# Kernel optimization log

Measured on AMD Instinct MI355X. Metric: run time of the kernel, lower is better.

Reference implementation:

```python
import math
import jax, jax.numpy as jnp
import numpy as np

E = 1024   # embed_dim
H = 16     # num_heads
DH = E // H
EPS = 1e-8

def round_ste(x):
    # straight-through round (matches brevitas STE behavior)
    return x + jax.lax.stop_gradient(jnp.round(x) - x)

def _scale(x, qmax):
    # dynamic per-tensor abs-max scale (stand-in for brevitas calibrated scale)
    return jnp.maximum(jnp.max(jnp.abs(x)) / qmax, EPS)

def fq(x, s, qmin, qmax):
    # fake-quantize: quantize to int grid, dequantize back to float
    return jnp.clip(round_ste(x / s), qmin, qmax) * s

def quant_linear(x, W, b):
    # Int8ActPerTensorFloat input, Int8WeightPerTensorFloat (narrow range) weight, Int32Bias
    s_x = _scale(x, 128.0)
    s_w = _scale(W, 127.0)
    xq = fq(x, s_x, -128, 127)
    wq = fq(W, s_w, -127, 127)
    y = xq @ wq.T
    if b is not None:
        s_b = s_x * s_w
        y = y + round_ste(b / s_b) * s_b
    return y

def setup_inputs() -> dict:
    k = jax.random.key(0)
    ks = jax.random.split(k, 7)
    S, B = 1024, 4
    return {
        "query": jax.random.normal(ks[0], (S, B, E), jnp.float32),
        "key": jax.random.normal(ks[1], (S, B, E), jnp.float32),
        "value": jax.random.normal(ks[2], (S, B, E), jnp.float32),
        "in_proj_weight": jax.random.normal(ks[3], (3 * E, E), jnp.float32) * 0.02,
        "in_proj_bias": jax.random.normal(ks[4], (3 * E,), jnp.float32) * 0.02,
        "out_proj_weight": jax.random.normal(ks[5], (E, E), jnp.float32) * 0.02,
        "out_proj_bias": jax.random.normal(ks[6], (E,), jnp.float32) * 0.02,
    }

def reference(query, key, value, in_proj_weight, in_proj_bias, out_proj_weight, out_proj_bias):
    S, B, _ = query.shape
    Wq, Wk, Wv = jnp.split(in_proj_weight, 3, axis=0)
    bq, bk, bv = jnp.split(in_proj_bias, 3)
    # quantized QKV projections (packed in_proj split per-input)
    q = quant_linear(query, Wq, bq)   # (S,B,E)
    k = quant_linear(key, Wk, bk)
    v = quant_linear(value, Wv, bv)

    def to_heads(x):  # (S,B,E) -> (B*H, S, DH)
        return x.reshape(S, B * H, DH).transpose(1, 0, 2)

    q = to_heads(q)
    k = to_heads(k)
    v = to_heads(v)

    # q_scaled quant (int8)
    q = q / math.sqrt(DH)
    q = fq(q, _scale(q, 128.0), -128, 127)
    # k_transposed quant (int8)
    kt = k.transpose(0, 2, 1)  # (B*H, DH, S)
    kt = fq(kt, _scale(kt, 128.0), -128, 127)

    attn = q @ kt                      # (B*H, S, S); softmax_input_quant=None -> identity
    attn = jax.nn.softmax(attn, axis=-1)
    # attn_output_weights quant (uint8)
    s_a = jnp.maximum(jnp.max(attn) / 255.0, EPS)
    attn = jnp.clip(round_ste(attn / s_a), 0, 255) * s_a
    # v quant (int8)
    v = fq(v, _scale(v, 128.0), -128, 127)

    out = attn @ v                     # (B*H, S, DH)
    out = out.transpose(1, 0, 2).reshape(S, B, E)
    out = quant_linear(out, out_proj_weight, out_proj_bias)
    return out
```

## Files before the change

### kernel.cpp

```cpp
#include <hip/hip_runtime.h>
#include <stdint.h>

typedef unsigned short u16;
typedef signed char i8;
typedef unsigned char u8;
typedef __attribute__((ext_vector_type(8))) short bf16x8;
typedef __attribute__((ext_vector_type(4))) float f32x4;
typedef __attribute__((ext_vector_type(4))) int i32x4;

#define S_LEN 1024
#define BATCH 4
#define EMB   1024
#define NH    16
#define DHEAD 64
#define BHEAD 64
#define NTOK  4096
#define KDIM  1024
#define NDIM  1024
#define EPSF  1e-8f
#define LOG2E 1.4426950408889634f

#define MFMAI8(a,b,c)  __builtin_amdgcn_mfma_i32_16x16x64_i8((a),(b),(c),0,0,0)

#define GLOAD16(g, l) __builtin_amdgcn_global_load_lds( \
    (const __attribute__((address_space(1))) void*)(g), \
    (__attribute__((address_space(3))) void*)(l), 16, 0, 0)

#define EXP2F(x) __builtin_amdgcn_exp2f(x)

__device__ __forceinline__ unsigned pack4(float a, float b, float c, float d){
  int qa = (int)a, qb = (int)b, qc = (int)c, qd = (int)d;
  return (unsigned)(qa & 255) | ((unsigned)(qb & 255) << 8) |
         ((unsigned)(qc & 255) << 16) | ((unsigned)(qd & 255) << 24);
}

__device__ __forceinline__ float wave_max(float v){
#pragma unroll
  for (int off = 32; off > 0; off >>= 1) v = fmaxf(v, __shfl_xor(v, off));
  return v;
}


__global__ __launch_bounds__(256) void k_zero(float* sc, int* vtot){
  if (blockIdx.x == 0){
    if (threadIdx.x < 16) sc[threadIdx.x] = 0.0f;
  } else {
    vtot[(blockIdx.x - 1)*256 + threadIdx.x] = 0;
  }
}

struct AQDesc { const float* x; u8* y; int n4; int slot; float qdiv; float lo; };
struct AQTable { AQDesc d[7]; };

__global__ __launch_bounds__(256) void k_absmax7(AQTable t, int* __restrict__ sci){
  const int bid = blockIdx.x;
  int seg, b0, nb;
  if (bid < 1536){ seg = bid >> 9; b0 = seg << 9; nb = 512; }
  else { seg = 3 + ((bid - 1536) >> 7); b0 = 1536 + ((seg - 3) << 7); nb = 128; }
  const AQDesc D = t.d[seg];
  const float4* x4 = (const float4*)D.x;
  const int base = (bid - b0)*256 + threadIdx.x;
  const int stride = nb*256;
  float4 v[8];
#pragma unroll
  for (int it = 0; it < 8; it++) v[it] = x4[base + it*stride];
  float m = 0.0f;
#pragma unroll
  for (int it = 0; it < 8; it++)
    m = fmaxf(m, fmaxf(fmaxf(fabsf(v[it].x), fabsf(v[it].y)),
                       fmaxf(fabsf(v[it].z), fabsf(v[it].w))));
  m = wave_max(m);
  __shared__ float red[4];
  int lane = threadIdx.x & 63, w = threadIdx.x >> 6;
  if (lane == 0) red[w] = m;
  __syncthreads();
  if (threadIdx.x == 0){
    float mm = fmaxf(fmaxf(red[0], red[1]), fmaxf(red[2], red[3]));
    atomicMax(sci + D.slot, __float_as_int(mm));
  }
}

__global__ __launch_bounds__(256) void k_quant7(AQTable t, const float* __restrict__ sc){
  const int bid = blockIdx.x;
  int seg, b0, nb;
  if (bid < 1536){ seg = bid >> 9; b0 = seg << 9; nb = 512; }
  else { seg = 3 + ((bid - 1536) >> 7); b0 = 1536 + ((seg - 3) << 7); nb = 128; }
  const AQDesc D = t.d[seg];
  const float s = fmaxf(sc[D.slot] / D.qdiv, EPSF);
  const float lo = D.lo;
  const float4* x4 = (const float4*)D.x;
  unsigned* y4 = (unsigned*)D.y;
  const int base = (bid - b0)*256 + threadIdx.x;
  const int stride = nb*256;
  float4 v[8];
#pragma unroll
  for (int it = 0; it < 8; it++) v[it] = x4[base + it*stride];
#pragma unroll
  for (int it = 0; it < 8; it++){
    float t0 = fminf(fmaxf(rintf(v[it].x / s), lo), 127.f);
    float t1 = fminf(fmaxf(rintf(v[it].y / s), lo), 127.f);
    float t2 = fminf(fmaxf(rintf(v[it].z / s), lo), 127.f);
    float t3 = fminf(fmaxf(rintf(v[it].w / s), lo), 127.f);
    y4[base + it*stride] = pack4(t0, t1, t2, t3);
  }
}

__global__ __launch_bounds__(256) void k_quant(const float* __restrict__ x,
    u8* __restrict__ y, const float* __restrict__ sc, int slot){
  const float s = fmaxf(sc[slot] / 128.0f, EPSF);
  const float4* x4 = (const float4*)x;
  unsigned* y4 = (unsigned*)y;
  const int base = blockIdx.x*256 + threadIdx.x;
  const int stride = 1024*256;
  float4 v[4];
#pragma unroll
  for (int it = 0; it < 4; it++) v[it] = x4[base + it*stride];
#pragma unroll
  for (int it = 0; it < 4; it++){
    float t0 = fminf(fmaxf(rintf(v[it].x / s), -128.f), 127.f);
    float t1 = fminf(fmaxf(rintf(v[it].y / s), -128.f), 127.f);
    float t2 = fminf(fmaxf(rintf(v[it].z / s), -128.f), 127.f);
    float t3 = fminf(fmaxf(rintf(v[it].w / s), -128.f), 127.f);
    y4[base + it*stride] = pack4(t0, t1, t2, t3);
  }
}

__device__ __forceinline__ void gemm_body(const i8* __restrict__ A,
    const i8* __restrict__ W, const float* __restrict__ bias,
    float* __restrict__ out, float s_b, int rowBase, int colBase,
    int* __restrict__ amax_out, i8 (*As)[128], i8 (*Bs)[128], float* red){
  const int tid = threadIdx.x;
  const int wid = tid >> 6, lane = tid & 63;
  const int wm = wid >> 2, wn = wid & 3;
  const int rr = lane & 15, g = lane >> 4;
  const int srow = wid*8 + (lane >> 3);
  const int sco  = ((lane & 7) ^ (lane >> 3)) << 4;
  const i8* Arow0 = &A[(size_t)(rowBase + srow)*KDIM + sco];
  const i8* Arow1 = &A[(size_t)(rowBase + 64 + srow)*KDIM + sco];
  const i8* Wrow0 = &W[(size_t)(colBase + srow)*KDIM + sco];
  const i8* Wrow1 = &W[(size_t)(colBase + 64 + srow)*KDIM + sco];
  i32x4 c[4][2] = {};
  int aoff[4][2], boff[2][2];
#pragma unroll
  for (int i = 0; i < 4; i++){
    int row = wm*64 + i*16 + rr;
#pragma unroll
    for (int h = 0; h < 2; h++)
      aoff[i][h] = row*128 + (((h*4 + g) ^ (row & 7)) << 4);
  }
#pragma unroll
  for (int j = 0; j < 2; j++){
    int row = wn*32 + j*16 + rr;
#pragma unroll
    for (int h = 0; h < 2; h++)
      boff[j][h] = row*128 + (((h*4 + g) ^ (row & 7)) << 4);
  }
  for (int k0 = 0; k0 < KDIM; k0 += 128){
    __syncthreads();
    GLOAD16(Arow0 + k0, &As[wid*8][0]);
    GLOAD16(Arow1 + k0, &As[64 + wid*8][0]);
    GLOAD16(Wrow0 + k0, &Bs[wid*8][0]);
    GLOAD16(Wrow1 + k0, &Bs[64 + wid*8][0]);
    __syncthreads();
#pragma unroll
    for (int h = 0; h < 2; h++){
      i32x4 af[4], bfr[2];
#pragma unroll
      for (int i = 0; i < 4; i++) af[i]  = *(const i32x4*)((const i8*)As + aoff[i][h]);
#pragma unroll
      for (int j = 0; j < 2; j++) bfr[j] = *(const i32x4*)((const i8*)Bs + boff[j][h]);
#pragma unroll
      for (int i = 0; i < 4; i++)
#pragma unroll
        for (int j = 0; j < 2; j++)
          c[i][j] = MFMAI8(af[i], bfr[j], c[i][j]);
    }
  }
  float lmax = 0.0f;
  const int r0 = (lane >> 4) * 4, ccol = lane & 15;
#pragma unroll
  for (int j = 0; j < 2; j++){
    int col = colBase + wn*32 + j*16 + ccol;
    float rb = rintf(bias[col] / s_b);
#pragma unroll
    for (int i = 0; i < 4; i++){
      int rowb = rowBase + wm*64 + i*16 + r0;
#pragma unroll
      for (int rI = 0; rI < 4; rI++){
        float y = s_b * ((float)c[i][j][rI] + rb);
        out[(size_t)(rowb + rI)*NDIM + col] = y;
        lmax = fmaxf(lmax, fabsf(y));
      }
    }
  }
  lmax = wave_max(lmax);
  if (lane == 0) red[wid] = lmax;
  __syncthreads();
  if (tid == 0){
    float mm = red[0];
#pragma unroll
    for (int i2 = 1; i2 < 8; i2++) mm = fmaxf(mm, red[i2]);
    atomicMax(amax_out, __float_as_int(mm));
  }
}

__global__ __launch_bounds__(512) void k_gemm3(const i8* __restrict__ Xall,
    const i8* __restrict__ Wall, const float* __restrict__ ball,
    float* __restrict__ Yall, const float* __restrict__ sc, int* __restrict__ sci){
  __shared__ i8 As[128][128];
  __shared__ i8 Bs[128][128];
  __shared__ float red[8];
  const int orig = blockIdx.x;
  const int xcd = orig & 7, sl = orig >> 3;
  const int seg = sl >> 5;
  const int t2 = xcd*32 + (sl & 31);
  const int by = t2 >> 3, bx = t2 & 7;
  const float s_x = fmaxf(sc[seg] / 128.0f, EPSF);
  const float s_w = fmaxf(sc[3 + seg] / 127.0f, EPSF);
  gemm_body(Xall + (size_t)seg*NTOK*KDIM, Wall + (size_t)seg*KDIM*NDIM,
            ball + seg*1024, Yall + (size_t)seg*NTOK*NDIM, s_x*s_w,
            by*128, bx*128, sci + 7 + seg, As, Bs, red);
}

__global__ __launch_bounds__(512) void k_gemm1(const i8* __restrict__ A,
    const i8* __restrict__ W, const float* __restrict__ bias,
    float* __restrict__ out, const float* __restrict__ sc,
    int sx_slot, int sw_slot, int* __restrict__ amax_out){
  __shared__ i8 As[128][128];
  __shared__ i8 Bs[128][128];
  __shared__ float red[8];
  const int orig = blockIdx.x;
  const int t2 = (orig & 7)*32 + (orig >> 3);
  const int by = t2 >> 3, bx = t2 & 7;
  const float s_x = fmaxf(sc[sx_slot] / 128.0f, EPSF);
  const float s_w = fmaxf(sc[sw_slot] / 127.0f, EPSF);
  gemm_body(A, W, bias, out, s_x*s_w, by*128, bx*128, amax_out, As, Bs, red);
}

__global__ __launch_bounds__(256) void k_quant_heads(const float* __restrict__ qf,
    const float* __restrict__ kf, const float* __restrict__ vf,
    i8* __restrict__ qh, i8* __restrict__ kh, i8* __restrict__ vt,
    int* __restrict__ vtot, const float* __restrict__ sc){
  const float s_q = fmaxf((sc[7]*0.125f)/128.0f, EPSF);
  const float s_k = fmaxf(sc[8]/128.0f, EPSF);
  const float s_v = fmaxf(sc[9]/128.0f, EPSF);
  __shared__ i8 tile[64][68];
  const int bx = blockIdx.x;
  const int st = bx & 15, hh = (bx >> 4) & 15, b = bx >> 8;
  const int t = threadIdx.x;
  const int sl = t >> 2, dc = (t & 3) * 16;
  const size_t row = (size_t)(st*64 + sl)*BATCH + b;
  const size_t ibase = row*EMB + hh*DHEAD + dc;
  const int bh = b*NH + hh;
  float vq[16], vk[16], vv[16];
#pragma unroll
  for (int i = 0; i < 4; i++){
    *(float4*)&vq[i*4] = *(const float4*)&qf[ibase + i*4];
    *(float4*)&vk[i*4] = *(const float4*)&kf[ibase + i*4];
    *(float4*)&vv[i*4] = *(const float4*)&vf[ibase + i*4];
  }
  alignas(16) i8 oq[16], ok[16];
#pragma unroll
  for (int i = 0; i < 16; i++){
    float tq = fminf(fmaxf(rintf((vq[i]*0.125f)/s_q), -128.f), 127.f);
    float tk = fminf(fmaxf(rintf(vk[i]/s_k), -128.f), 127.f);
    float tv = fminf(fmaxf(rintf(vv[i]/s_v), -128.f), 127.f);
    oq[i] = (i8)(int)tq; ok[i] = (i8)(int)tk;
    tile[dc + i][sl] = (i8)(int)tv;
  }
  const size_t qoff = ((size_t)bh*S_LEN + st*64 + sl)*DHEAD + dc;
  *(int4*)&qh[qoff] = *(const int4*)&oq[0];
  *(int4*)&kh[qoff] = *(const int4*)&ok[0];
  __syncthreads();
  const int d = t >> 2, sc4 = (t & 3) * 16;
  int ovi[4];
  int sum = 0;
#pragma unroll
  for (int w4 = 0; w4 < 4; w4++){
    unsigned x = *(const unsigned*)&tile[d][sc4 + w4*4];
    ovi[w4] = (int)x;
#pragma unroll
    for (int bb = 0; bb < 4; bb++) sum += (int)(i8)(x >> (8*bb));
  }
  const size_t voff = ((size_t)bh*DHEAD + d)*S_LEN + st*64 + sc4;
  *(int4*)&vt[voff] = *(const int4*)&ovi[0];
  sum += __shfl_xor(sum, 1);
  sum += __shfl_xor(sum, 2);
  if ((t & 3) == 0) atomicAdd(&vtot[bh*DHEAD + d], sum);
}

__global__ __launch_bounds__(256) void k_attn1(const i8* __restrict__ qh,
    const i8* __restrict__ kh, float* __restrict__ mrow, float* __restrict__ lrow,
    const float* __restrict__ sc, int* __restrict__ sci){
  __shared__ i8 Ks[128][64];
  __shared__ float red2[4];
  const int orig = blockIdx.x;
  const int tile = (orig & 7) * 128 + (orig >> 3);
  const int bhead = tile >> 4, q0 = (tile & 15) * 64;
  const int tid = threadIdx.x, w = tid >> 6, lane = tid & 63;
  const int rr = lane & 15, g = lane >> 4;
  const float s_q = fmaxf((sc[7]*0.125f)/128.0f, EPSF);
  const float s_k = fmaxf(sc[8]/128.0f, EPSF);
  const float C1 = s_q * s_k * LOG2E;
  const i8* qbase = qh + ((size_t)bhead*S_LEN + q0 + w*16)*DHEAD;
  const i8* kbase = kh + (size_t)bhead*S_LEN*DHEAD;
  i32x4 a = *(const i32x4*)&qbase[rr*DHEAD + g*16];
  const int ksel = ((lane & 3) ^ ((lane >> 3) & 3)) << 4;
  const int kr = lane >> 2;
  float m = -1e30f, l = 0.0f;
  for (int cch = 0; cch < 8; cch++){
    const int n0 = cch * 128;
    __syncthreads();
    GLOAD16(&kbase[(size_t)(n0 + w*32 + kr)*DHEAD + ksel],      &Ks[w*32][0]);
    GLOAD16(&kbase[(size_t)(n0 + w*32 + 16 + kr)*DHEAD + ksel], &Ks[w*32 + 16][0]);
    __syncthreads();
    float sv[8][4];
#pragma unroll
    for (int nt = 0; nt < 8; nt++){
      int row = nt*16 + rr;
      i32x4 b = *(const i32x4*)((const i8*)Ks + row*64 + (((g ^ ((row >> 1) & 3))) << 4));
      i32x4 acc = {};
      acc = MFMAI8(b, a, acc);
#pragma unroll
      for (int r = 0; r < 4; r++) sv[nt][r] = (float)acc[r]*C1;
    }
    float cm = sv[0][0];
#pragma unroll
    for (int nt = 0; nt < 8; nt++)
#pragma unroll
      for (int r = 0; r < 4; r++) cm = fmaxf(cm, sv[nt][r]);
    float mn = fmaxf(m, cm);
    l *= EXP2F(m - mn);
    m = mn;
#pragma unroll
    for (int nt = 0; nt < 8; nt++)
#pragma unroll
      for (int r = 0; r < 4; r++) l += EXP2F(sv[nt][r] - m);
  }
#pragma unroll
  for (int off = 16; off < 64; off <<= 1){
    float mo = __shfl_xor(m, off), lo = __shfl_xor(l, off);
    float mn = fmaxf(m, mo);
    l = l*EXP2F(m - mn) + lo*EXP2F(mo - mn);
    m = mn;
  }
  if (g == 0){
    mrow[(size_t)bhead*S_LEN + q0 + w*16 + rr] = m;
    lrow[(size_t)bhead*S_LEN + q0 + w*16 + rr] = l;
  }
  float im = wave_max(1.0f / l);
  if (lane == 0) red2[w] = im;
  __syncthreads();
  if (tid == 0){
    float mm = fmaxf(fmaxf(red2[0], red2[1]), fmaxf(red2[2], red2[3]));
    atomicMax(sci + 13, __float_as_int(mm));
  }
}

__global__ __launch_bounds__(256) void k_attn2(const i8* __restrict__ qh,
    const i8* __restrict__ kh, const i8* __restrict__ vt,
    const float* __restrict__ mrow, const float* __restrict__ lrow,
    const int* __restrict__ vtot, float* __restrict__ aout,
    const float* __restrict__ sc, const int* __restrict__ sci,
    int* __restrict__ amax_out){
  __shared__ i8 Ks[128][64];
  __shared__ i8 Vs[64][128];
  __shared__ i8 P[4][16][136];
  __shared__ float red[4];
  const int orig = blockIdx.x;
  const int tile = (orig & 7) * 128 + (orig >> 3);
  const int bhead = tile >> 4, q0 = (tile & 15) * 64;
  const int tid = threadIdx.x, w = tid >> 6, lane = tid & 63;
  const int rr = lane & 15, g = lane >> 4;
  const float s_q = fmaxf((sc[7]*0.125f)/128.0f, EPSF);
  const float s_k = fmaxf(sc[8]/128.0f, EPSF);
  const float C1 = s_q * s_k * LOG2E;
  const float s_v = fmaxf(sc[9]/128.0f, EPSF);
  const float s_a = fmaxf(__int_as_float(sci[13]) / 255.0f, EPSF);
  const float fac = s_a * s_v;
  const i8* qbase = qh + ((size_t)bhead*S_LEN + q0 + w*16)*DHEAD;
  const i8* kbase = kh + (size_t)bhead*S_LEN*DHEAD;
  const i8* vbase = vt + (size_t)bhead*DHEAD*S_LEN;
  i32x4 a = *(const i32x4*)&qbase[rr*DHEAD + g*16];
  float nb;
  {
    size_t qr = (size_t)bhead*S_LEN + q0 + w*16 + rr;
    float inv = 1.0f / (lrow[qr] * s_a);
    nb = log2f(inv) - mrow[qr];
  }
  const int ksel = ((lane & 3) ^ ((lane >> 3) & 3)) << 4;
  const int kr = lane >> 2;
  const int vsel = (((lane & 7) ^ ((lane >> 3) & 7)) << 4);
  const int vr = lane >> 3;
  i32x4 cpv[4] = {};
  for (int cch = 0; cch < 8; cch++){
    const int n0 = cch * 128;
    __syncthreads();
    GLOAD16(&kbase[(size_t)(n0 + w*32 + kr)*DHEAD + ksel],      &Ks[w*32][0]);
    GLOAD16(&kbase[(size_t)(n0 + w*32 + 16 + kr)*DHEAD + ksel], &Ks[w*32 + 16][0]);
    GLOAD16(&vbase[(size_t)(w*16 + vr)*S_LEN + n0 + vsel],      &Vs[w*16][0]);
    GLOAD16(&vbase[(size_t)(w*16 + 8 + vr)*S_LEN + n0 + vsel],  &Vs[w*16 + 8][0]);
    __syncthreads();
#pragma unroll
    for (int nt = 0; nt < 8; nt++){
      int row = nt*16 + rr;
      i32x4 b = *(const i32x4*)((const i8*)Ks + row*64 + (((g ^ ((row >> 1) & 3))) << 4));
      i32x4 acc = {};
      acc = MFMAI8(b, a, acc);
      float er0 = fminf(rintf(EXP2F(fmaf((float)acc[0], C1, nb))), 255.0f);
      float er1 = fminf(rintf(EXP2F(fmaf((float)acc[1], C1, nb))), 255.0f);
      float er2 = fminf(rintf(EXP2F(fmaf((float)acc[2], C1, nb))), 255.0f);
      float er3 = fminf(rintf(EXP2F(fmaf((float)acc[3], C1, nb))), 255.0f);
      unsigned pw;
      asm("v_cvt_pk_u8_f32 %0, %1, 0, 0"  : "=v"(pw) : "v"(er0));
      asm("v_cvt_pk_u8_f32 %0, %1, 1, %0" : "+v"(pw) : "v"(er1));
      asm("v_cvt_pk_u8_f32 %0, %1, 2, %0" : "+v"(pw) : "v"(er2));
      asm("v_cvt_pk_u8_f32 %0, %1, 3, %0" : "+v"(pw) : "v"(er3));
      pw ^= 0x80808080u;
      *(unsigned*)&P[w][rr][nt*16 + g*4] = pw;
    }
#pragma unroll
    for (int h = 0; h < 2; h++){
      i32x4 pa;
      {
        const i8* pptr = &P[w][rr][h*64 + g*16];
        pa[0] = *(const int*)(pptr + 0);
        pa[1] = *(const int*)(pptr + 4);
        pa[2] = *(const int*)(pptr + 8);
        pa[3] = *(const int*)(pptr + 12);
      }
#pragma unroll
      for (int f = 0; f < 4; f++){
        int row = f*16 + rr;
        i32x4 bv = *(const i32x4*)((const i8*)Vs + row*128 + (((h*4 + g) ^ (row & 7)) << 4));
        cpv[f] = MFMAI8(pa, bv, cpv[f]);
      }
    }
  }
  const int b = bhead >> 4, hh = bhead & 15;
  float lmax = 0.0f;
#pragma unroll
  for (int f = 0; f < 4; f++){
    int d = f*16 + rr;
    int vcorr = 128 * vtot[bhead*DHEAD + d];
#pragma unroll
    for (int r = 0; r < 4; r++){
      int srow2 = q0 + w*16 + g*4 + r;
      float y = fac * (float)(cpv[f][r] + vcorr);
      aout[(size_t)(srow2*BATCH + b)*EMB + hh*DHEAD + d] = y;
      lmax = fmaxf(lmax, fabsf(y));
    }
  }
  lmax = wave_max(lmax);
  __syncthreads();
  if (lane == 0) red[w] = lmax;
  __syncthreads();
  if (tid == 0){
    float mm = fmaxf(fmaxf(red[0], red[1]), fmaxf(red[2], red[3]));
    atomicMax(amax_out, __float_as_int(mm));
  }
}

extern "C" void kernel_launch(void* const* d_in, const int* in_sizes, int n_in,
                              void* d_out, int out_size, void* d_ws, size_t ws_size,
                              hipStream_t stream){
  const float* query = (const float*)d_in[0];
  const float* key   = (const float*)d_in[1];
  const float* value = (const float*)d_in[2];
  const float* inW   = (const float*)d_in[3];
  const float* inB   = (const float*)d_in[4];
  const float* outW  = (const float*)d_in[5];
  const float* outB  = (const float*)d_in[6];
  float* out = (float*)d_out;

  char* ws = (char*)d_ws;
  float* sc  = (float*)ws;
  int*   sci = (int*)ws;
  int*   vtotI = (int*)(ws + 256);
  u8* WQQ = (u8*)(ws + 256 + 16384);
  u8* WKQ = WQQ + 1024*1024;
  u8* WVQ = WKQ + 1024*1024;
  u8* WOQ = WVQ + 1024*1024;
  u8* XQ  = WOQ + 1024*1024;
  u8* XK  = XQ + (size_t)NTOK*1024;
  u8* XV  = XK + (size_t)NTOK*1024;
  float* QF = (float*)(XV + (size_t)NTOK*1024);
  float* KF = QF + (size_t)NTOK*1024;
  float* VF = KF + (size_t)NTOK*1024;
  i8* VT = (i8*)(VF + (size_t)NTOK*1024);
  float* MROW = (float*)(VT + (size_t)BHEAD*DHEAD*S_LEN);
  float* LROW = MROW + BHEAD*S_LEN;
  i8* QH  = (i8*)XQ;   i8* KH = (i8*)XK;
  float* AOUT = QF;
  u8* AOQ = XV;

  AQTable tab;
  tab.d[0] = { query,             XQ,  NTOK*1024/4, 0, 128.f, -128.f };
  tab.d[1] = { key,               XK,  NTOK*1024/4, 1, 128.f, -128.f };
  tab.d[2] = { value,             XV,  NTOK*1024/4, 2, 128.f, -128.f };
  tab.d[3] = { inW,               WQQ, 1024*1024/4, 3, 127.f, -127.f };
  tab.d[4] = { inW + 1024*1024,   WKQ, 1024*1024/4, 4, 127.f, -127.f };
  tab.d[5] = { inW + 2*1024*1024, WVQ, 1024*1024/4, 5, 127.f, -127.f };
  tab.d[6] = { outW,              WOQ, 1024*1024/4, 6, 127.f, -127.f };

  k_zero<<<17, 256, 0, stream>>>(sc, vtotI);
  k_absmax7<<<2048, 256, 0, stream>>>(tab, sci);
  k_quant7<<<2048, 256, 0, stream>>>(tab, sc);
  k_gemm3<<<768, 512, 0, stream>>>((const i8*)XQ, (const i8*)WQQ, inB, QF, sc, sci);
  k_quant_heads<<<1024, 256, 0, stream>>>(QF, KF, VF, QH, KH, VT, vtotI, sc);
  k_attn1<<<1024, 256, 0, stream>>>(QH, KH, MROW, LROW, sc, sci);
  k_attn2<<<1024, 256, 0, stream>>>(QH, KH, VT, MROW, LROW, vtotI, AOUT, sc, sci, sci + 10);
  k_quant<<<1024, 256, 0, stream>>>(AOUT, AOQ, sc, 10);
  k_gemm1<<<256, 512, 0, stream>>>((const i8*)AOQ, (const i8*)WOQ, outB, out, sc, 10, 6, sci + 12);
}
```

Before: 177.8 us.

## Register-prefetch next K/V chunk in attention kernels instead of direct LDS loads

Replaces the global_load_lds direct-to-LDS copies of K and V tiles in both attention passes with register loads that fetch the next chunk while the current chunk is computed, then store into LDS at the top of the next iteration. This overlaps global memory latency with MFMA and exp work, removing the stall between the two barriers. It costs extra VGPRs for the staging registers and extra LDS store instructions, which may lower occupancy.

```diff
diff --git a/kernel.cpp b/kernel.cpp
--- a/kernel.cpp
+++ b/kernel.cpp
@@ -307,13 +307,19 @@
   i32x4 a = *(const i32x4*)&qbase[rr*DHEAD + g*16];
   const int ksel = ((lane & 3) ^ ((lane >> 3) & 3)) << 4;
   const int kr = lane >> 2;
+  i8* kdst = (i8*)Ks + w*2048 + lane*16;
+  int4 rk0 = *(const int4*)&kbase[(size_t)(w*32 + kr)*DHEAD + ksel];
+  int4 rk1 = *(const int4*)&kbase[(size_t)(w*32 + 16 + kr)*DHEAD + ksel];
   float m = -1e30f, l = 0.0f;
   for (int cch = 0; cch < 8; cch++){
-    const int n0 = cch * 128;
+    *(int4*)kdst          = rk0;
+    *(int4*)(kdst + 1024) = rk1;
     __syncthreads();
-    GLOAD16(&kbase[(size_t)(n0 + w*32 + kr)*DHEAD + ksel],      &Ks[w*32][0]);
-    GLOAD16(&kbase[(size_t)(n0 + w*32 + 16 + kr)*DHEAD + ksel], &Ks[w*32 + 16][0]);
-    __syncthreads();
+    if (cch < 7){
+      const int n1 = (cch + 1) * 128;
+      rk0 = *(const int4*)&kbase[(size_t)(n1 + w*32 + kr)*DHEAD + ksel];
+      rk1 = *(const int4*)&kbase[(size_t)(n1 + w*32 + 16 + kr)*DHEAD + ksel];
+    }
     float sv[8][4];
 #pragma unroll
     for (int nt = 0; nt < 8; nt++){
@@ -336,6 +342,7 @@
     for (int nt = 0; nt < 8; nt++)
 #pragma unroll
       for (int r = 0; r < 4; r++) l += EXP2F(sv[nt][r] - m);
+    __syncthreads();
   }
 #pragma unroll
   for (int off = 16; off < 64; off <<= 1){
@@ -392,15 +399,26 @@
   const int kr = lane >> 2;
   const int vsel = (((lane & 7) ^ ((lane >> 3) & 7)) << 4);
   const int vr = lane >> 3;
+  i8* kdst = (i8*)Ks + w*2048 + lane*16;
+  i8* vdst = (i8*)Vs + w*2048 + lane*16;
+  int4 rk0 = *(const int4*)&kbase[(size_t)(w*32 + kr)*DHEAD + ksel];
+  int4 rk1 = *(const int4*)&kbase[(size_t)(w*32 + 16 + kr)*DHEAD + ksel];
+  int4 rv0 = *(const int4*)&vbase[(size_t)(w*16 + vr)*S_LEN + vsel];
+  int4 rv1 = *(const int4*)&vbase[(size_t)(w*16 + 8 + vr)*S_LEN + vsel];
   i32x4 cpv[4] = {};
   for (int cch = 0; cch < 8; cch++){
-    const int n0 = cch * 128;
+    *(int4*)kdst          = rk0;
+    *(int4*)(kdst + 1024) = rk1;
+    *(int4*)vdst          = rv0;
+    *(int4*)(vdst + 1024) = rv1;
     __syncthreads();
-    GLOAD16(&kbase[(size_t)(n0 + w*32 + kr)*DHEAD + ksel],      &Ks[w*32][0]);
-    GLOAD16(&kbase[(size_t)(n0 + w*32 + 16 + kr)*DHEAD + ksel], &Ks[w*32 + 16][0]);
-    GLOAD16(&vbase[(size_t)(w*16 + vr)*S_LEN + n0 + vsel],      &Vs[w*16][0]);
-    GLOAD16(&vbase[(size_t)(w*16 + 8 + vr)*S_LEN + n0 + vsel],  &Vs[w*16 + 8][0]);
-    __syncthreads();
+    if (cch < 7){
+      const int n1 = (cch + 1) * 128;
+      rk0 = *(const int4*)&kbase[(size_t)(n1 + w*32 + kr)*DHEAD + ksel];
+      rk1 = *(const int4*)&kbase[(size_t)(n1 + w*32 + 16 + kr)*DHEAD + ksel];
+      rv0 = *(const int4*)&vbase[(size_t)(w*16 + vr)*S_LEN + n1 + vsel];
+      rv1 = *(const int4*)&vbase[(size_t)(w*16 + 8 + vr)*S_LEN + n1 + vsel];
+    }
 #pragma unroll
     for (int nt = 0; nt < 8; nt++){
       int row = nt*16 + rr;
@@ -436,6 +454,7 @@
         cpv[f] = MFMAI8(pa, bv, cpv[f]);
       }
     }
+    __syncthreads();
   }
   const int b = bhead >> 4, hh = bhead & 15;
   float lmax = 0.0f;
```

Result: faster. 173.2 us, median of 2 (-2.6%).
